# Optimization experiments

Hardware: AMD Instinct MI355X
Metric: run time of the kernel (lower is better)

Reference implementation:

```python
import jax, jax.numpy as jnp
import numpy as np

B, S, IN, OUT = 4, 2048, 4096, 11008

def setup_inputs() -> dict:
    key = jax.random.key(0)
    k1, k2, k3, k4, k5 = jax.random.split(key, 5)
    x = jax.random.normal(k1, (B, S, IN), dtype=jnp.float32)
    # int8-range quantized weight stored as int32 for portability
    weight = jax.random.randint(k2, (OUT, IN), 0, 256, dtype=jnp.int32) - 128
    scale = (jax.random.uniform(k3, (OUT, 1), dtype=jnp.float32) * 0.01 + 1e-4).astype(jnp.float16)
    zp = jax.random.randint(k4, (OUT, 1), 0, 256, dtype=jnp.int32) - 128
    bias = jax.random.normal(k5, (OUT,), dtype=jnp.float32) * 0.02
    return {"x": x, "weight": weight, "scale": scale, "zp": zp, "bias": bias}

def reference(x, weight, scale, zp, bias):
    dtype = x.dtype
    # per-row dequant: (w_q - zp) * scale, then F.linear(x, w_rec, bias)
    w_rec = (weight.astype(dtype) - zp.astype(dtype)) * scale.astype(dtype)  # [OUT, IN]
    return jnp.einsum('bsi,oi->bso', x, w_rec) + bias
```

## Files before the change

kernel.cpp:

```cpp
#include <hip/hip_runtime.h>
#include <hip/hip_bf16.h>


#define MDIM 8192
#define NDIM 11008
#define KDIM 4096

#define BM 256
#define BN 256
#define BK 64
#define KT (KDIM / BK)
#define NTM (MDIM / BM)
#define NTN (NDIM / BN)
#define NWG (NTM * NTN)

typedef signed char i8;
typedef int i32x4 __attribute__((ext_vector_type(4)));


__global__ void conv_w8(const int* __restrict__ w, i8* __restrict__ w8) {
    const size_t e = ((size_t)blockIdx.x * 256 + threadIdx.x) << 4;
    const int4 a = *(const int4*)(w + e);
    const int4 b = *(const int4*)(w + e + 4);
    const int4 c = *(const int4*)(w + e + 8);
    const int4 d = *(const int4*)(w + e + 12);
    i8 q[16];
    q[0] = (i8)a.x; q[1] = (i8)a.y; q[2] = (i8)a.z; q[3] = (i8)a.w;
    q[4] = (i8)b.x; q[5] = (i8)b.y; q[6] = (i8)b.z; q[7] = (i8)b.w;
    q[8] = (i8)c.x; q[9] = (i8)c.y; q[10] = (i8)c.z; q[11] = (i8)c.w;
    q[12] = (i8)d.x; q[13] = (i8)d.y; q[14] = (i8)d.z; q[15] = (i8)d.w;
    *(int4*)(w8 + e) = *(const int4*)q;
}

__global__ __launch_bounds__(256) void conv_xq(const float* __restrict__ x,
                                               i8* __restrict__ xq,
                                               float* __restrict__ sx,
                                               float* __restrict__ xs) {
    __shared__ float ramax[4], rsum[4];
    const int row = blockIdx.x;
    const float* xr = x + (size_t)row * KDIM;
    const int t = threadIdx.x;
    const float4* p = (const float4*)xr + (t << 2);
    float4 v0 = p[0], v1 = p[1], v2 = p[2], v3 = p[3];
    float amax = 0.f, sum = 0.f;
    float vv[16] = {v0.x, v0.y, v0.z, v0.w, v1.x, v1.y, v1.z, v1.w,
                    v2.x, v2.y, v2.z, v2.w, v3.x, v3.y, v3.z, v3.w};
#pragma unroll
    for (int i = 0; i < 16; ++i) {
        amax = fmaxf(amax, fabsf(vv[i]));
        sum += vv[i];
    }
#pragma unroll
    for (int off = 32; off > 0; off >>= 1) {
        amax = fmaxf(amax, __shfl_down(amax, off, 64));
        sum += __shfl_down(sum, off, 64);
    }
    if ((t & 63) == 0) { ramax[t >> 6] = amax; rsum[t >> 6] = sum; }
    __syncthreads();
    amax = fmaxf(fmaxf(ramax[0], ramax[1]), fmaxf(ramax[2], ramax[3]));
    sum = (rsum[0] + rsum[1]) + (rsum[2] + rsum[3]);
    const float inv = (amax > 0.f) ? 127.0f / amax : 0.f;
    if (t == 0) {
        sx[row] = amax * (1.0f / 127.0f);
        xs[row] = sum;
    }
    i8 q[16];
#pragma unroll
    for (int i = 0; i < 16; ++i) q[i] = (i8)(int)rintf(vv[i] * inv);
    *(int4*)(xq + (size_t)row * KDIM + (t << 4)) = *(const int4*)q;
}


__device__ __forceinline__ void gload16(const i8* g, i8* l) {
    __builtin_amdgcn_global_load_lds(
        (const __attribute__((address_space(1))) unsigned int*)g,
        (__attribute__((address_space(3))) unsigned int*)l, 16, 0, 0);
}

#define STAGE_A(T) do { const int _s = (T) & 3; const int _k = (T) * BK;          \
    gload16(gA0 + _k, &SH[_s][0][wid * 1024]);                                    \
    gload16(gA1 + _k, &SH[_s][0][8192 + wid * 1024]); } while (0)
#define STAGE_B(T) do { const int _s = (T) & 3; const int _k = (T) * BK;          \
    gload16(gB0 + _k, &SH[_s][1][wid * 1024]);                                    \
    gload16(gB1 + _k, &SH[_s][1][8192 + wid * 1024]); } while (0)

#define GROUP(T, DO_STAGE, WAITOP) do {                                           \
    const i8* _sA = &SH[(T) & 3][0][0];                                           \
    const i8* _sB = &SH[(T) & 3][1][0];                                           \
    i32x4 aF[4], bF[4], aG[4];                                                    \
    _Pragma("unroll") for (int _f = 0; _f < 4; ++_f) {                            \
        aF[_f] = *(const i32x4*)(_sA + aoff + _f * 1024);                         \
        bF[_f] = *(const i32x4*)(_sB + boff + _f * 1024);                         \
    }                                                                             \
    if (DO_STAGE) STAGE_A((T) + 3);                                               \
    __builtin_amdgcn_s_barrier();                                                 \
    __builtin_amdgcn_s_setprio(1);                                                \
    _Pragma("unroll") for (int _i = 0; _i < 4; ++_i)                              \
    _Pragma("unroll") for (int _j = 0; _j < 4; ++_j)                              \
        acc[_i][_j] = __builtin_amdgcn_mfma_i32_16x16x64_i8(                      \
            aF[_i], bF[_j], acc[_i][_j], 0, 0, 0);                                \
    __builtin_amdgcn_s_setprio(0);                                                \
    __builtin_amdgcn_s_barrier();                                                 \
    _Pragma("unroll") for (int _f = 0; _f < 4; ++_f)                              \
        aG[_f] = *(const i32x4*)(_sA + aoff + (_f + 4) * 1024);                   \
    if (DO_STAGE) STAGE_B((T) + 3);                                               \
    __builtin_amdgcn_s_barrier();                                                 \
    __builtin_amdgcn_s_setprio(1);                                                \
    _Pragma("unroll") for (int _i = 0; _i < 4; ++_i)                              \
    _Pragma("unroll") for (int _j = 0; _j < 4; ++_j)                              \
        acc[_i + 4][_j] = __builtin_amdgcn_mfma_i32_16x16x64_i8(                  \
            aG[_i], bF[_j], acc[_i + 4][_j], 0, 0, 0);                            \
    __builtin_amdgcn_s_setprio(0);                                                \
    WAITOP;                                                                       \
    __builtin_amdgcn_s_barrier();                                                 \
} while (0)

__global__ __launch_bounds__(512, 2) void gemm_q(const i8* __restrict__ Xq,
                                                 const i8* __restrict__ Wq,
                                                 const float* __restrict__ sx,
                                                 const float* __restrict__ xs,
                                                 const float* __restrict__ scale,
                                                 const int* __restrict__ zp,
                                                 const float* __restrict__ bias,
                                                 float* __restrict__ out) {
    __shared__ __align__(16) i8 SH[4][2][16384];

    const int tid = threadIdx.x;
    const int wid = tid >> 6;
    const int lane = tid & 63;

    const int bid = blockIdx.x;
    const int pm = ((bid & 7) << 2) | ((bid >> 3) & 3);
    const int pn = bid >> 5;
    const int bm0 = pm * BM;
    const int bn0 = pn * BN;

    const int srow = tid >> 2;
    const int scol = ((tid & 3) << 4) ^ (((tid >> 5) & 1) << 5);
    const i8* gA0 = Xq + (size_t)(bm0 + srow) * KDIM + scol;
    const i8* gA1 = gA0 + (size_t)128 * KDIM;
    const i8* gB0 = Wq + (size_t)(bn0 + srow) * KDIM + scol;
    const i8* gB1 = gB0 + (size_t)128 * KDIM;

    const int wm = wid >> 2, wn = wid & 3;
    const int lr = lane & 15;
    const int kb = (lane >> 4) << 4;
    const int swz = (lr & 8) << 2;
    const int aoff = (((wm * 128 + lr) << 6) + kb) ^ swz;
    const int boff = (((wn * 64 + lr) << 6) + kb) ^ swz;

    i32x4 acc[8][4];
#pragma unroll
    for (int i = 0; i < 8; ++i)
#pragma unroll
        for (int j = 0; j < 4; ++j) acc[i][j] = (i32x4){0, 0, 0, 0};

    STAGE_A(0); STAGE_B(0);
    STAGE_A(1); STAGE_B(1);
    STAGE_A(2); STAGE_B(2);
    asm volatile("s_waitcnt vmcnt(8)" ::: "memory");
    __builtin_amdgcn_s_barrier();

    for (int t = 0; t < KT - 3; ++t) {
        GROUP(t, true, asm volatile("s_waitcnt vmcnt(8)" ::: "memory"));
    }
    GROUP(KT - 3, false, asm volatile("s_waitcnt vmcnt(4)" ::: "memory"));
    GROUP(KT - 2, false, asm volatile("s_waitcnt vmcnt(0)" ::: "memory"));
    GROUP(KT - 1, false, (void)0);

    const int rr = (lane >> 4) << 2;
#pragma unroll
    for (int j = 0; j < 4; ++j) {
        const int n = bn0 + wn * 64 + j * 16 + lr;
        const float sc = scale[n];
        const float zpn = (float)zp[n];
        const float bi = bias[n];
#pragma unroll
        for (int i = 0; i < 8; ++i) {
            const int m = bm0 + wm * 128 + i * 16 + rr;
#pragma unroll
            for (int r = 0; r < 4; ++r) {
                const int mm = m + r;
                const float d = (float)acc[i][j][r];
                out[(size_t)mm * NDIM + n] = sc * (sx[mm] * d - zpn * xs[mm]) + bi;
            }
        }
    }
}


__global__ void naive_q(const float* __restrict__ x, const int* __restrict__ wq,
                        const float* __restrict__ scale, const int* __restrict__ zp,
                        const float* __restrict__ bias, float* __restrict__ out) {
    const long long idx = (long long)blockIdx.x * 256 + threadIdx.x;
    if (idx >= (long long)MDIM * NDIM) return;
    const int m = (int)(idx / NDIM);
    const int n = (int)(idx % NDIM);
    const float* xr = x + (long long)m * KDIM;
    const int* wr = wq + (long long)n * KDIM;
    float dot = 0.f, xsum = 0.f;
    for (int k = 0; k < KDIM; ++k) {
        dot += xr[k] * (float)wr[k];
        xsum += xr[k];
    }
    out[idx] = scale[n] * (dot - (float)zp[n] * xsum) + bias[n];
}

extern "C" void kernel_launch(void* const* d_in, const int* in_sizes, int n_in,
                              void* d_out, int out_size, void* d_ws, size_t ws_size,
                              hipStream_t stream) {
    const float* x = (const float*)d_in[0];
    const int* wq = (const int*)d_in[1];
    const float* scale = (const float*)d_in[2];
    const int* zp = (const int*)d_in[3];
    const float* bias = (const float*)d_in[4];
    float* out = (float*)d_out;

    const size_t w8_bytes = (size_t)NDIM * KDIM;
    const size_t xq_bytes = (size_t)MDIM * KDIM;
    const size_t row_bytes = (size_t)MDIM * 4;
    const size_t need = w8_bytes + xq_bytes + 2 * row_bytes;

    if (ws_size >= need) {
        i8* w8 = (i8*)d_ws;
        i8* xq8 = (i8*)((char*)d_ws + w8_bytes);
        float* sx = (float*)((char*)d_ws + w8_bytes + xq_bytes);
        float* xs = (float*)((char*)d_ws + w8_bytes + xq_bytes + row_bytes);
        conv_w8<<<(unsigned)(w8_bytes / 16 / 256), 256, 0, stream>>>(wq, w8);
        conv_xq<<<MDIM, 256, 0, stream>>>(x, xq8, sx, xs);
        gemm_q<<<NWG, 512, 0, stream>>>(xq8, w8, sx, xs, scale, zp, bias, out);
    } else {
        const long long total = (long long)MDIM * NDIM;
        naive_q<<<(unsigned)((total + 255) / 256), 256, 0, stream>>>(
            x, wq, scale, zp, bias, out);
    }
}
```

Baseline: 565.8 us.

## Halve N tile to 128, triple-buffer LDS and raise occupancy target

Shrinks the workgroup tile from 256x256 to 256x128 and remaps the 8 waves into a 4x2 grid of 64x64 sub-tiles. The LDS pipeline drops from four 32KB stages to three 24KB stages, prefetching two K-steps ahead instead of three, with the vmcnt waits adjusted to match. Launch bounds now target 4 blocks per CU. The aim is more workgroups and more resident waves to hide latency, at the cost of less operand reuse per tile, twice as many tiles, and a shallower prefetch.

```diff
diff --git a/kernel.cpp b/kernel.cpp
--- a/kernel.cpp
+++ b/kernel.cpp
@@ -7,12 +7,15 @@
 #define KDIM 4096
 
 #define BM 256
-#define BN 256
+#define BN 128
 #define BK 64
 #define KT (KDIM / BK)
 #define NTM (MDIM / BM)
 #define NTN (NDIM / BN)
 #define NWG (NTM * NTN)
+
+#define SLOT 24576
+#define BOFFS 16384
 
 typedef signed char i8;
 typedef int i32x4 __attribute__((ext_vector_type(4)));
@@ -77,45 +80,44 @@
         (__attribute__((address_space(3))) unsigned int*)l, 16, 0, 0);
 }
 
-#define STAGE_A(T) do { const int _s = (T) & 3; const int _k = (T) * BK;          \
-    gload16(gA0 + _k, &SH[_s][0][wid * 1024]);                                    \
-    gload16(gA1 + _k, &SH[_s][0][8192 + wid * 1024]); } while (0)
-#define STAGE_B(T) do { const int _s = (T) & 3; const int _k = (T) * BK;          \
-    gload16(gB0 + _k, &SH[_s][1][wid * 1024]);                                    \
-    gload16(gB1 + _k, &SH[_s][1][8192 + wid * 1024]); } while (0)
+#define STAGE_A(T) do { const int _s = (T) % 3; const int _k = (T) * BK;          \
+    gload16(gA0 + _k, &SH[_s][wid * 1024]);                                       \
+    gload16(gA1 + _k, &SH[_s][8192 + wid * 1024]); } while (0)
+#define STAGE_B(T) do { const int _s = (T) % 3; const int _k = (T) * BK;          \
+    gload16(gB0 + _k, &SH[_s][BOFFS + wid * 1024]); } while (0)
 
 #define GROUP(T, DO_STAGE, WAITOP) do {                                           \
-    const i8* _sA = &SH[(T) & 3][0][0];                                           \
-    const i8* _sB = &SH[(T) & 3][1][0];                                           \
-    i32x4 aF[4], bF[4], aG[4];                                                    \
-    _Pragma("unroll") for (int _f = 0; _f < 4; ++_f) {                            \
+    const i8* _sA = &SH[(T) % 3][0];                                              \
+    const i8* _sB = &SH[(T) % 3][BOFFS];                                          \
+    i32x4 aF[2], bF[4], aG[2];                                                    \
+    _Pragma("unroll") for (int _f = 0; _f < 2; ++_f)                              \
         aF[_f] = *(const i32x4*)(_sA + aoff + _f * 1024);                         \
+    _Pragma("unroll") for (int _f = 0; _f < 4; ++_f)                              \
         bF[_f] = *(const i32x4*)(_sB + boff + _f * 1024);                         \
-    }                                                                             \
-    if (DO_STAGE) STAGE_A((T) + 3);                                               \
+    if (DO_STAGE) STAGE_A((T) + 2);                                               \
     __builtin_amdgcn_s_barrier();                                                 \
     __builtin_amdgcn_s_setprio(1);                                                \
-    _Pragma("unroll") for (int _i = 0; _i < 4; ++_i)                              \
+    _Pragma("unroll") for (int _i = 0; _i < 2; ++_i)                              \
     _Pragma("unroll") for (int _j = 0; _j < 4; ++_j)                              \
         acc[_i][_j] = __builtin_amdgcn_mfma_i32_16x16x64_i8(                      \
             aF[_i], bF[_j], acc[_i][_j], 0, 0, 0);                                \
     __builtin_amdgcn_s_setprio(0);                                                \
     __builtin_amdgcn_s_barrier();                                                 \
-    _Pragma("unroll") for (int _f = 0; _f < 4; ++_f)                              \
-        aG[_f] = *(const i32x4*)(_sA + aoff + (_f + 4) * 1024);                   \
-    if (DO_STAGE) STAGE_B((T) + 3);                                               \
+    _Pragma("unroll") for (int _f = 0; _f < 2; ++_f)                              \
+        aG[_f] = *(const i32x4*)(_sA + aoff + (_f + 2) * 1024);                   \
+    if (DO_STAGE) STAGE_B((T) + 2);                                               \
     __builtin_amdgcn_s_barrier();                                                 \
     __builtin_amdgcn_s_setprio(1);                                                \
-    _Pragma("unroll") for (int _i = 0; _i < 4; ++_i)                              \
+    _Pragma("unroll") for (int _i = 0; _i < 2; ++_i)                              \
     _Pragma("unroll") for (int _j = 0; _j < 4; ++_j)                              \
-        acc[_i + 4][_j] = __builtin_amdgcn_mfma_i32_16x16x64_i8(                  \
-            aG[_i], bF[_j], acc[_i + 4][_j], 0, 0, 0);                            \
+        acc[_i + 2][_j] = __builtin_amdgcn_mfma_i32_16x16x64_i8(                  \
+            aG[_i], bF[_j], acc[_i + 2][_j], 0, 0, 0);                            \
     __builtin_amdgcn_s_setprio(0);                                                \
     WAITOP;                                                                       \
     __builtin_amdgcn_s_barrier();                                                 \
 } while (0)
 
-__global__ __launch_bounds__(512, 2) void gemm_q(const i8* __restrict__ Xq,
+__global__ __launch_bounds__(512, 4) void gemm_q(const i8* __restrict__ Xq,
                                                  const i8* __restrict__ Wq,
                                                  const float* __restrict__ sx,
                                                  const float* __restrict__ xs,
@@ -123,15 +125,16 @@
                                                  const int* __restrict__ zp,
                                                  const float* __restrict__ bias,
                                                  float* __restrict__ out) {
-    __shared__ __align__(16) i8 SH[4][2][16384];
+    __shared__ __align__(16) i8 SH[3][SLOT];
 
     const int tid = threadIdx.x;
     const int wid = tid >> 6;
     const int lane = tid & 63;
 
     const int bid = blockIdx.x;
-    const int pm = ((bid & 7) << 2) | ((bid >> 3) & 3);
-    const int pn = bid >> 5;
+    const int off = bid >> 3;
+    const int pm = ((bid & 7) << 2) | (off & 3);
+    const int pn = off >> 2;
     const int bm0 = pm * BM;
     const int bn0 = pn * BN;
 
@@ -140,31 +143,28 @@
     const i8* gA0 = Xq + (size_t)(bm0 + srow) * KDIM + scol;
     const i8* gA1 = gA0 + (size_t)128 * KDIM;
     const i8* gB0 = Wq + (size_t)(bn0 + srow) * KDIM + scol;
-    const i8* gB1 = gB0 + (size_t)128 * KDIM;
-
-    const int wm = wid >> 2, wn = wid & 3;
+
+    const int wm = wid >> 1, wn = wid & 1;
     const int lr = lane & 15;
     const int kb = (lane >> 4) << 4;
     const int swz = (lr & 8) << 2;
-    const int aoff = (((wm * 128 + lr) << 6) + kb) ^ swz;
+    const int aoff = (((wm * 64 + lr) << 6) + kb) ^ swz;
     const int boff = (((wn * 64 + lr) << 6) + kb) ^ swz;
 
-    i32x4 acc[8][4];
-#pragma unroll
-    for (int i = 0; i < 8; ++i)
+    i32x4 acc[4][4];
+#pragma unroll
+    for (int i = 0; i < 4; ++i)
 #pragma unroll
         for (int j = 0; j < 4; ++j) acc[i][j] = (i32x4){0, 0, 0, 0};
 
     STAGE_A(0); STAGE_B(0);
     STAGE_A(1); STAGE_B(1);
-    STAGE_A(2); STAGE_B(2);
-    asm volatile("s_waitcnt vmcnt(8)" ::: "memory");
+    asm volatile("s_waitcnt vmcnt(3)" ::: "memory");
     __builtin_amdgcn_s_barrier();
 
-    for (int t = 0; t < KT - 3; ++t) {
-        GROUP(t, true, asm volatile("s_waitcnt vmcnt(8)" ::: "memory"));
-    }
-    GROUP(KT - 3, false, asm volatile("s_waitcnt vmcnt(4)" ::: "memory"));
+    for (int t = 0; t < KT - 2; ++t) {
+        GROUP(t, true, asm volatile("s_waitcnt vmcnt(3)" ::: "memory"));
+    }
     GROUP(KT - 2, false, asm volatile("s_waitcnt vmcnt(0)" ::: "memory"));
     GROUP(KT - 1, false, (void)0);
 
@@ -176,8 +176,8 @@
         const float zpn = (float)zp[n];
         const float bi = bias[n];
 #pragma unroll
-        for (int i = 0; i < 8; ++i) {
-            const int m = bm0 + wm * 128 + i * 16 + rr;
+        for (int i = 0; i < 4; ++i) {
+            const int m = bm0 + wm * 64 + i * 16 + rr;
 #pragma unroll
             for (int r = 0; r < 4; ++r) {
                 const int mm = m + r;
```

After: 545.5 us. 3.6% less time.
